# Kernel tuning notes

Hardware: AMD Instinct MI355X
Metric: run time of the kernel (lower is better)

## Reference

```python
import jax, jax.numpy as jnp
import numpy as np

N = 4_194_304
B = 64
H = 16
TAU = 1.0


def setup_inputs() -> dict:
    key = jax.random.key(0)
    ks = jax.random.split(key, 8)
    pos = jax.random.normal(ks[0], (N, 3), dtype=jnp.float32)
    reflectance = jax.random.uniform(ks[1], (N,), dtype=jnp.float32)
    batch = jnp.sort(jax.random.randint(ks[2], (N,), 0, B).astype(jnp.int32))
    gumbels = jax.random.gumbel(ks[3], (B, 2), dtype=jnp.float32)
    W1 = jax.random.normal(ks[4], (4, H), dtype=jnp.float32) * 0.5
    b1 = jnp.zeros((H,), dtype=jnp.float32)
    W2 = jax.random.normal(ks[5], (H, H), dtype=jnp.float32) * 0.25
    b2 = jnp.zeros((H,), dtype=jnp.float32)
    Wg = jax.random.normal(ks[6], (H, 2), dtype=jnp.float32) * 0.25
    bg = jnp.array([0.0, 2.0], dtype=jnp.float32)  # gate_nn bias init per module
    return {"pos": pos, "reflectance": reflectance, "batch": batch, "gumbels": gumbels,
            "W1": W1, "b1": b1, "W2": W2, "b2": b2, "Wg": Wg, "bg": bg}


def reference(pos, reflectance, batch, gumbels, W1, b1, W2, b2, Wg, bg):
    # point-wise MLP: [N,4] -> [N,H]
    features = jnp.concatenate([pos, reflectance[:, None]], axis=-1)
    h = jax.nn.relu(features @ W1 + b1)
    h = jax.nn.relu(h @ W2 + b2)
    # batch-indexed max pool: [N,H] -> [B,H]
    sample_features = jax.ops.segment_max(h, batch, num_segments=B)
    gate_logits = sample_features @ Wg + bg  # [B,2]
    # gumbel-softmax (hard=False as in forward)
    gate_decision = jax.nn.softmax((gate_logits + gumbels) / TAU, axis=-1)
    # gather per-point gate and scale reflectance
    use_reflectance = gate_decision[:, 1][batch]  # [N]
    return use_reflectance * reflectance
```

## Files before the change

kernel.cpp:

```cpp
#include <hip/hip_runtime.h>
#include <hip/hip_bf16.h>


#define N_PTS 4194304
#define NB 64
#define NH 16
#define WPB 4
#define SITERS 4
#define PTW (256 * SITERS)
#define PPB (WPB * PTW)
#define NBLK (N_PTS / PPB)
#define NENT (NBLK * 2)

typedef __attribute__((ext_vector_type(8))) short bf16x8;
typedef __attribute__((ext_vector_type(4))) float f32x4;
union U8 { bf16x8 v; unsigned u[4]; unsigned short s[8]; };

struct Rec { int idA, idB, bpos; };

__device__ __forceinline__ unsigned pk2(float a, float b) {
    float2 t; t.x = a; t.y = b;
    __hip_bfloat162 r = __float22bfloat162_rn(t);
    unsigned u;
    __builtin_memcpy(&u, &r, sizeof(u));
    return u;
}
__device__ __forceinline__ unsigned short f2bf(float x) {
    unsigned u = __float_as_uint(x);
    u = u + 0x7fffu + ((u >> 16) & 1u);
    return (unsigned short)(u >> 16);
}

template<bool SLOW>
__device__ __forceinline__ void do_chunk(
    const float4& q0, const float4& q1, const float4& q2, const float4& rr,
    int sb, int g, int col, int bposw,
    const U8& A1, const U8& A2, const f32x4& c1, const f32x4& c2,
    f32x4& accA, f32x4& accB)
{
    const float f[4][4] = {{q0.x, q0.y, q0.z, rr.x},
                           {q0.w, q1.x, q1.y, rr.y},
                           {q1.z, q1.w, q2.x, rr.z},
                           {q2.y, q2.z, q2.w, rr.w}};
#pragma unroll
    for (int j = 0; j < 4; ++j) {
        const unsigned F01 = pk2(f[j][0], f[j][1]);
        const unsigned F23 = pk2(f[j][2], f[j][3]);
        f32x4 d[4], h[4];
#pragma unroll
        for (int t = 0; t < 4; ++t) {
            const bool mine = (g == t);
            U8 B;
            B.u[0] = mine ? F01 : 0u;
            B.u[1] = mine ? F23 : 0u;
            B.u[2] = 0u; B.u[3] = 0u;
            d[t] = __builtin_amdgcn_mfma_f32_16x16x32_bf16(A1.v, B.v, c1, 0, 0, 0);
        }
#pragma unroll
        for (int t = 0; t < 4; ++t) {
            U8 P;
            P.u[0] = pk2(fmaxf(d[t][0], 0.f), fmaxf(d[t][1], 0.f));
            P.u[1] = pk2(fmaxf(d[t][2], 0.f), fmaxf(d[t][3], 0.f));
            P.u[2] = 0u; P.u[3] = 0u;
            h[t] = __builtin_amdgcn_mfma_f32_16x16x32_bf16(A2.v, P.v, c2, 0, 0, 0);
        }
#pragma unroll
        for (int t = 0; t < 4; ++t) {
            if (!SLOW) {
#pragma unroll
                for (int r = 0; r < 4; ++r) accA[r] = fmaxf(accA[r], h[t][r]);
            } else {
                const bool m = (sb + 4 * (16 * t + col) + j) < bposw;
#pragma unroll
                for (int r = 0; r < 4; ++r) {
                    accA[r] = fmaxf(accA[r], m ? h[t][r] : 0.f);
                    accB[r] = fmaxf(accB[r], m ? 0.f : h[t][r]);
                }
            }
        }
    }
}

__global__ __launch_bounds__(256, 4) void mlp_segmax_kernel(
    const float* __restrict__ pos,
    const float* __restrict__ refl,
    const int*   __restrict__ batch,
    const float* __restrict__ W1, const float* __restrict__ b1,
    const float* __restrict__ W2, const float* __restrict__ b2,
    float* __restrict__ pv,
    int*   __restrict__ pid,
    Rec*   __restrict__ recs)
{
    __shared__ float lv[WPB][2][NH];
    __shared__ int   li[WPB][2];
    __shared__ int   lbp[WPB];

    const int lane = threadIdx.x & 63;
    const int wid  = threadIdx.x >> 6;
    const int col  = lane & 15;
    const int g    = lane >> 4;
    const int wb   = (blockIdx.x * WPB + wid) * PTW;

    U8 A1, A2;
#pragma unroll
    for (int e = 0; e < 4; ++e) {
        A1.s[e]     = f2bf(W1[e * NH + col]);
        A1.s[e + 4] = 0;
        A2.s[e]     = f2bf(W2[(4 * g + e) * NH + col]);
        A2.s[e + 4] = 0;
    }
    f32x4 c1, c2;
#pragma unroll
    for (int r = 0; r < 4; ++r) { c1[r] = b1[4 * g + r]; c2[r] = b2[4 * g + r]; }

    const int idA = batch[wb];
    const int idB = batch[wb + PTW - 1];
    const bool isSlow = (idA != idB);

    f32x4 accA = {0.f, 0.f, 0.f, 0.f};
    f32x4 accB = {0.f, 0.f, 0.f, 0.f};

    const float4* gp = (const float4*)(pos + (size_t)wb * 3);
    const float4* gr = (const float4*)(refl + wb);

    float4 q0 = gp[3 * lane + 0];
    float4 q1 = gp[3 * lane + 1];
    float4 q2 = gp[3 * lane + 2];
    float4 rr = gr[lane];

    if (!isSlow) {
#pragma unroll
        for (int s = 0; s < SITERS; ++s) {
            float4 n0, n1, n2, nr;
            if (s + 1 < SITERS) {
                n0 = gp[(s + 1) * 192 + 3 * lane + 0];
                n1 = gp[(s + 1) * 192 + 3 * lane + 1];
                n2 = gp[(s + 1) * 192 + 3 * lane + 2];
                nr = gr[(s + 1) * 64 + lane];
            }
            do_chunk<false>(q0, q1, q2, rr, wb + s * 256, g, col, 0,
                            A1, A2, c1, c2, accA, accB);
            if (s + 1 < SITERS) { q0 = n0; q1 = n1; q2 = n2; rr = nr; }
        }
    } else {
        int bposw = 0x7fffffff;
        for (int it = 0; it < PTW / 64; ++it) {
            const int idx = wb + it * 64 + lane;
            const unsigned long long mk = __ballot(batch[idx] != idA);
            if (mk) bposw = min(bposw, wb + it * 64 + (__ffsll((long long)mk) - 1));
        }
#pragma unroll
        for (int s = 0; s < SITERS; ++s) {
            float4 n0, n1, n2, nr;
            if (s + 1 < SITERS) {
                n0 = gp[(s + 1) * 192 + 3 * lane + 0];
                n1 = gp[(s + 1) * 192 + 3 * lane + 1];
                n2 = gp[(s + 1) * 192 + 3 * lane + 2];
                nr = gr[(s + 1) * 64 + lane];
            }
            do_chunk<true>(q0, q1, q2, rr, wb + s * 256, g, col, bposw,
                           A1, A2, c1, c2, accA, accB);
            if (s + 1 < SITERS) { q0 = n0; q1 = n1; q2 = n2; rr = nr; }
        }
        lbp[wid] = bposw;
    }

#pragma unroll
    for (int mk = 1; mk <= 8; mk <<= 1) {
#pragma unroll
        for (int r = 0; r < 4; ++r) {
            accA[r] = fmaxf(accA[r], __shfl_xor(accA[r], mk));
            accB[r] = fmaxf(accB[r], __shfl_xor(accB[r], mk));
        }
    }
    if (col == 0) {
        *reinterpret_cast<float4*>(&lv[wid][0][4 * g]) =
            make_float4(accA[0], accA[1], accA[2], accA[3]);
        *reinterpret_cast<float4*>(&lv[wid][1][4 * g]) =
            make_float4(accB[0], accB[1], accB[2], accB[3]);
    }
    if (lane == 0) {
        li[wid][0] = idA; li[wid][1] = idB;
        if (!isSlow) lbp[wid] = 0x7fffffff;
    }
    __syncthreads();

    if (threadIdx.x < NH) {
        const int d   = threadIdx.x;
        const int ida = li[0][0];
        const int idb = li[WPB - 1][1];
        float mA = 0.f, mB = 0.f;
#pragma unroll
        for (int s = 0; s < WPB; ++s)
#pragma unroll
            for (int hh = 0; hh < 2; ++hh) {
                const float val = lv[s][hh][d];
                if (li[s][hh] == ida) mA = fmaxf(mA, val);
                else                  mB = fmaxf(mB, val);
            }
        pv[(blockIdx.x * 2 + 0) * NH + d] = mA;
        pv[(blockIdx.x * 2 + 1) * NH + d] = mB;
        if (d == 0) {
            pid[blockIdx.x * 2 + 0] = ida;
            pid[blockIdx.x * 2 + 1] = idb;
            int bp = 0x7fffffff;
#pragma unroll
            for (int s = 0; s < WPB; ++s) {
                if (li[s][0] != ida) bp = min(bp, (int)(blockIdx.x * PPB + s * PTW));
                else if (lbp[s] != 0x7fffffff) bp = min(bp, lbp[s]);
            }
            Rec r; r.idA = ida; r.idB = idb; r.bpos = bp;
            recs[blockIdx.x] = r;
        }
    }
}

__global__ __launch_bounds__(1024) void stage2_kernel(
    const float* __restrict__ pv, const int* __restrict__ pid,
    const float* __restrict__ Wg, const float* __restrict__ bg,
    const float* __restrict__ gum, float* __restrict__ gate)
{
    __shared__ unsigned int sm[NB * NH];
    const int tid = threadIdx.x;
    sm[tid] = 0u;
    __syncthreads();

    for (int i = tid; i < NENT * 4; i += 1024) {
        const float4 v = reinterpret_cast<const float4*>(pv)[i];
        const int e  = i >> 2;
        const int d0 = (i & 3) * 4;
        const int id = pid[e];
        atomicMax(&sm[id * NH + d0 + 0], __float_as_uint(v.x));
        atomicMax(&sm[id * NH + d0 + 1], __float_as_uint(v.y));
        atomicMax(&sm[id * NH + d0 + 2], __float_as_uint(v.z));
        atomicMax(&sm[id * NH + d0 + 3], __float_as_uint(v.w));
    }
    __syncthreads();

    if (tid < NB) {
        float l0 = bg[0] + gum[tid * 2 + 0];
        float l1 = bg[1] + gum[tid * 2 + 1];
#pragma unroll
        for (int k = 0; k < NH; ++k) {
            const float s = __uint_as_float(sm[tid * NH + k]);
            l0 = fmaf(s, Wg[k * 2 + 0], l0);
            l1 = fmaf(s, Wg[k * 2 + 1], l1);
        }
        gate[tid] = 1.f / (1.f + expf(-(l1 - l0)));
    }
}

__global__ __launch_bounds__(256) void scale_kernel(
    const float* __restrict__ refl,
    const Rec*   __restrict__ recs,
    const float* __restrict__ gate,
    float* __restrict__ out)
{
    const Rec rec = recs[blockIdx.x >> 2];
    const float gA = gate[rec.idA];
    const float gB = gate[rec.idB];

    const int p0 = (blockIdx.x * 256 + threadIdx.x) * 4;
    const float4 rr = *reinterpret_cast<const float4*>(refl + p0);
    float4 o;
    o.x = ((p0 + 0) < rec.bpos ? gA : gB) * rr.x;
    o.y = ((p0 + 1) < rec.bpos ? gA : gB) * rr.y;
    o.z = ((p0 + 2) < rec.bpos ? gA : gB) * rr.z;
    o.w = ((p0 + 3) < rec.bpos ? gA : gB) * rr.w;
    *reinterpret_cast<float4*>(out + p0) = o;
}

extern "C" void kernel_launch(void* const* d_in, const int* in_sizes, int n_in,
                              void* d_out, int out_size, void* d_ws, size_t ws_size,
                              hipStream_t stream) {
    const float* pos   = (const float*)d_in[0];
    const float* refl  = (const float*)d_in[1];
    const int*   batch = (const int*)d_in[2];
    const float* gumb  = (const float*)d_in[3];
    const float* W1    = (const float*)d_in[4];
    const float* b1    = (const float*)d_in[5];
    const float* W2    = (const float*)d_in[6];
    const float* b2    = (const float*)d_in[7];
    const float* Wg    = (const float*)d_in[8];
    const float* bg    = (const float*)d_in[9];
    float* out = (float*)d_out;

    float* pv   = (float*)d_ws;
    int*   pid  = (int*)((char*)d_ws + 131072);
    Rec*   recs = (Rec*)((char*)d_ws + 139264);
    float* gate = (float*)((char*)d_ws + 151552);

    mlp_segmax_kernel<<<NBLK, 256, 0, stream>>>(pos, refl, batch,
                                                W1, b1, W2, b2, pv, pid, recs);
    stage2_kernel<<<1, 1024, 0, stream>>>(pv, pid, Wg, bg, gumb, gate);
    scale_kernel<<<N_PTS / 1024, 256, 0, stream>>>(refl, recs, gate, out);
}
```

Measured before the change: 40.24 us.

## Fuse gate computation into scale kernel and stage MLP weights through LDS

The single-block stage2 kernel is removed. Each scale block now scans all partial-max entries, keeps only those whose ids match its own two batch ids, reduces them into LDS and computes its own two sigmoid gates before scaling reflectance. This drops one kernel launch and the serialized single-block reduction, but every one of the 4096 scale blocks now reads the full pid array (2048 ints) plus the matching pv rows, which adds redundant L2 traffic. Separately, the MLP kernel loads W1/b1/W2/b2 cooperatively into shared memory instead of having each lane issue scattered global loads.

```diff
diff --git a/kernel.cpp b/kernel.cpp
--- a/kernel.cpp
+++ b/kernel.cpp
@@ -91,27 +91,38 @@
     int*   __restrict__ pid,
     Rec*   __restrict__ recs)
 {
+    __shared__ float wlds[352];
     __shared__ float lv[WPB][2][NH];
     __shared__ int   li[WPB][2];
     __shared__ int   lbp[WPB];
 
-    const int lane = threadIdx.x & 63;
-    const int wid  = threadIdx.x >> 6;
+    const int tid  = threadIdx.x;
+    const int lane = tid & 63;
+    const int wid  = tid >> 6;
     const int col  = lane & 15;
     const int g    = lane >> 4;
     const int wb   = (blockIdx.x * WPB + wid) * PTW;
 
+    if (tid < 64)  wlds[tid]        = W1[tid];
+    if (tid < 16)  wlds[64 + tid]   = b1[tid];
+    wlds[80 + tid] = W2[tid];
+    if (tid < 16)  wlds[336 + tid]  = b2[tid];
+    __syncthreads();
+
     U8 A1, A2;
 #pragma unroll
     for (int e = 0; e < 4; ++e) {
-        A1.s[e]     = f2bf(W1[e * NH + col]);
+        A1.s[e]     = f2bf(wlds[e * NH + col]);
         A1.s[e + 4] = 0;
-        A2.s[e]     = f2bf(W2[(4 * g + e) * NH + col]);
+        A2.s[e]     = f2bf(wlds[80 + (4 * g + e) * NH + col]);
         A2.s[e + 4] = 0;
     }
     f32x4 c1, c2;
 #pragma unroll
-    for (int r = 0; r < 4; ++r) { c1[r] = b1[4 * g + r]; c2[r] = b2[4 * g + r]; }
+    for (int r = 0; r < 4; ++r) {
+        c1[r] = wlds[64 + 4 * g + r];
+        c2[r] = wlds[336 + 4 * g + r];
+    }
 
     const int idA = batch[wb];
     const int idB = batch[wb + PTW - 1];
@@ -185,8 +196,8 @@
     }
     __syncthreads();
 
-    if (threadIdx.x < NH) {
-        const int d   = threadIdx.x;
+    if (tid < NH) {
+        const int d   = tid;
         const int ida = li[0][0];
         const int idb = li[WPB - 1][1];
         float mA = 0.f, mB = 0.f;
@@ -215,58 +226,74 @@
     }
 }
 
-__global__ __launch_bounds__(1024) void stage2_kernel(
-    const float* __restrict__ pv, const int* __restrict__ pid,
+__global__ __launch_bounds__(256) void gate_scale_kernel(
+    const float* __restrict__ refl,
+    const float* __restrict__ pv,
+    const int*   __restrict__ pid,
+    const Rec*   __restrict__ recs,
     const float* __restrict__ Wg, const float* __restrict__ bg,
-    const float* __restrict__ gum, float* __restrict__ gate)
+    const float* __restrict__ gum,
+    float* __restrict__ out)
 {
-    __shared__ unsigned int sm[NB * NH];
+    __shared__ unsigned smA[NH], smB[NH];
+    __shared__ unsigned short list[128];
+    __shared__ unsigned cnt;
+    __shared__ float gAB[2];
+
     const int tid = threadIdx.x;
-    sm[tid] = 0u;
-    __syncthreads();
-
-    for (int i = tid; i < NENT * 4; i += 1024) {
-        const float4 v = reinterpret_cast<const float4*>(pv)[i];
-        const int e  = i >> 2;
-        const int d0 = (i & 3) * 4;
-        const int id = pid[e];
-        atomicMax(&sm[id * NH + d0 + 0], __float_as_uint(v.x));
-        atomicMax(&sm[id * NH + d0 + 1], __float_as_uint(v.y));
-        atomicMax(&sm[id * NH + d0 + 2], __float_as_uint(v.z));
-        atomicMax(&sm[id * NH + d0 + 3], __float_as_uint(v.w));
-    }
-    __syncthreads();
-
-    if (tid < NB) {
-        float l0 = bg[0] + gum[tid * 2 + 0];
-        float l1 = bg[1] + gum[tid * 2 + 1];
+    const Rec rec = recs[blockIdx.x >> 2];
+
+    if (tid < NH) { smA[tid] = 0u; smB[tid] = 0u; }
+    if (tid == 0) cnt = 0u;
+    __syncthreads();
+
+#pragma unroll
+    for (int k = 0; k < NENT / 256; ++k) {
+        const int e = k * 256 + tid;
+        const int p = pid[e];
+        const bool a = (p == rec.idA);
+        const bool b = (p == rec.idB) && !a;
+        if (a || b) {
+            const unsigned i = atomicAdd(&cnt, 1u);
+            if (i < 128u) list[i] = (unsigned short)(e | (a ? 0 : 0x8000));
+        }
+    }
+    __syncthreads();
+
+    const int n = (int)(cnt < 128u ? cnt : 128u);
+    for (int k = tid; k < n * NH; k += 256) {
+        const int i = k >> 4, d = k & 15;
+        const int e = list[i] & 0x7fff;
+        unsigned* dst = (list[i] & 0x8000) ? smB : smA;
+        atomicMax(dst + d, __float_as_uint(pv[e * NH + d]));
+    }
+    __syncthreads();
+
+    if (tid < 2) {
+        const int bsel = tid ? rec.idB : rec.idA;
+        const unsigned* sm = tid ? smB : smA;
+        float l0 = bg[0] + gum[bsel * 2 + 0];
+        float l1 = bg[1] + gum[bsel * 2 + 1];
 #pragma unroll
         for (int k = 0; k < NH; ++k) {
-            const float s = __uint_as_float(sm[tid * NH + k]);
+            const float s = __uint_as_float(sm[k]);
             l0 = fmaf(s, Wg[k * 2 + 0], l0);
             l1 = fmaf(s, Wg[k * 2 + 1], l1);
         }
-        gate[tid] = 1.f / (1.f + expf(-(l1 - l0)));
-    }
-}
-
-__global__ __launch_bounds__(256) void scale_kernel(
-    const float* __restrict__ refl,
-    const Rec*   __restrict__ recs,
-    const float* __restrict__ gate,
-    float* __restrict__ out)
-{
-    const Rec rec = recs[blockIdx.x >> 2];
-    const float gA = gate[rec.idA];
-    const float gB = gate[rec.idB];
-
-    const int p0 = (blockIdx.x * 256 + threadIdx.x) * 4;
-    const float4 rr = *reinterpret_cast<const float4*>(refl + p0);
+        gAB[tid] = 1.f / (1.f + expf(-(l1 - l0)));
+    }
+    __syncthreads();
+
+    const float gA = gAB[0];
+    const float gB = (rec.idA == rec.idB) ? gAB[0] : gAB[1];
+
+    const int p0 = (blockIdx.x * 256 + tid) * 4;
+    const float4 rv = *reinterpret_cast<const float4*>(refl + p0);
     float4 o;
-    o.x = ((p0 + 0) < rec.bpos ? gA : gB) * rr.x;
-    o.y = ((p0 + 1) < rec.bpos ? gA : gB) * rr.y;
-    o.z = ((p0 + 2) < rec.bpos ? gA : gB) * rr.z;
-    o.w = ((p0 + 3) < rec.bpos ? gA : gB) * rr.w;
+    o.x = ((p0 + 0) < rec.bpos ? gA : gB) * rv.x;
+    o.y = ((p0 + 1) < rec.bpos ? gA : gB) * rv.y;
+    o.z = ((p0 + 2) < rec.bpos ? gA : gB) * rv.z;
+    o.w = ((p0 + 3) < rec.bpos ? gA : gB) * rv.w;
     *reinterpret_cast<float4*>(out + p0) = o;
 }
 
@@ -288,10 +315,9 @@
     float* pv   = (float*)d_ws;
     int*   pid  = (int*)((char*)d_ws + 131072);
     Rec*   recs = (Rec*)((char*)d_ws + 139264);
-    float* gate = (float*)((char*)d_ws + 151552);
 
     mlp_segmax_kernel<<<NBLK, 256, 0, stream>>>(pos, refl, batch,
                                                 W1, b1, W2, b2, pv, pid, recs);
-    stage2_kernel<<<1, 1024, 0, stream>>>(pv, pid, Wg, bg, gumb, gate);
-    scale_kernel<<<N_PTS / 1024, 256, 0, stream>>>(refl, recs, gate, out);
-}
+    gate_scale_kernel<<<N_PTS / 1024, 256, 0, stream>>>(refl, pv, pid, recs,
+                                                        Wg, bg, gumb, out);
+}
```

After: 38.98 us, median of 2. 3.1% less time.
